# Performance work log

Measured on AMD Instinct MI355X. Metric: run time of the kernel, lower is better.

The kernel has to match this reference:

```python
import jax, jax.numpy as jnp
import numpy as np
from jax import lax

HEADS = 8
HEAD_C = 16  # attention_channels // heads = 128 // 8


def setup_inputs() -> dict:
    key = jax.random.key(0)
    ks = jax.random.split(key, 16)
    N, I, H, W = 8, 128, 36, 36
    R, C, A, O = 128, 128, 128, 128  # recurrent, common, attention, out channels
    s = lambda *sh: 0.05
    inp = {
        'x': jax.random.normal(ks[0], (N, I, H, W), jnp.float32),
        # input 1x1 conv (Accumulate of single Conv, bias init 0)
        'w_in': jax.random.normal(ks[1], (R, I), jnp.float32) * 0.05,
        'b_in': jnp.zeros((R,), jnp.float32),
        # 3x3 conv on cat([x, h]) -> common channels
        'w_conv': jax.random.normal(ks[2], (C, 2 * R, 3, 3), jnp.float32) * 0.05,
        'b_conv': jnp.zeros((C,), jnp.float32),
        # q/k/v 1x1 projections (no bias)
        'wq': jax.random.normal(ks[3], (A, C), jnp.float32) * 0.05,
        'wk': jax.random.normal(ks[4], (A, C), jnp.float32) * 0.05,
        'wv': jax.random.normal(ks[5], (A, C), jnp.float32) * 0.05,
        # gate 1x1 projections on cat([z, a]) (C + A inputs)
        'w_i': jax.random.normal(ks[6], (R, C + A), jnp.float32) * 0.05,
        'b_i': jnp.full((R,), -1.0, jnp.float32),  # init_input
        'w_f': jax.random.normal(ks[7], (R, C + A), jnp.float32) * 0.05,
        'b_f': jnp.full((R,), 1.0, jnp.float32),   # init_forget
        'w_g': jax.random.normal(ks[8], (R, C + A), jnp.float32) * 0.05,
        'b_g': jnp.zeros((R,), jnp.float32),
        'w_o': jax.random.normal(ks[9], (R, C + A), jnp.float32) * 0.05,
        'b_o': jnp.zeros((R,), jnp.float32),
        # output 1x1 conv
        'w_out': jax.random.normal(ks[10], (O, R), jnp.float32) * 0.05,
        'b_out': jnp.zeros((O,), jnp.float32),
    }
    return inp


def _conv1x1(w, x, b=None):
    y = jnp.einsum('oi,nihw->nohw', w, x)
    if b is not None:
        y = y + b[None, :, None, None]
    return y


def reference(x, w_in, b_in, w_conv, b_conv, wq, wk, wv,
              w_i, b_i, w_f, b_f, w_g, b_g, w_o, b_o, w_out, b_out):
    # first timestep: past is empty -> h = c = 0
    xt = jnp.tanh(_conv1x1(w_in, x, b_in))          # [N, R, H, W]
    h0 = jnp.zeros_like(xt)
    c0 = jnp.zeros_like(xt)
    xh = jnp.concatenate([xt, h0], axis=1)          # groups=1 -> plain concat
    z = lax.conv_general_dilated(xh, w_conv, (1, 1), 'SAME') + b_conv[None, :, None, None]
    N, C, H, W = z.shape
    HW = H * W
    q = _conv1x1(wq, z).reshape(N, HEADS, HEAD_C, HW)
    k = _conv1x1(wk, z).reshape(N, HEADS, HEAD_C, HW)
    v = _conv1x1(wv, z).reshape(N, HEADS, HEAD_C, HW)
    # spatial attention over H*W tokens per head
    w_attn = jax.nn.softmax(jnp.einsum('nhcq,nhcd->nhqd', q, k), axis=-1)  # [N,heads,HW,HW]
    a = jnp.einsum('nhcd,nhqd->nhcq', v, w_attn).reshape(N, -1, H, W)      # [N,A,H,W]
    za = jnp.concatenate([z, a], axis=1)
    i = jax.nn.sigmoid(_conv1x1(w_i, za, b_i))
    f = jax.nn.sigmoid(_conv1x1(w_f, za, b_f))
    g = jnp.tanh(_conv1x1(w_g, za, b_g))
    o = jax.nn.sigmoid(_conv1x1(w_o, za, b_o))
    c = f * c0 + i * g
    h = o * jnp.tanh(c)  # dropout p=0 -> identity
    return _conv1x1(w_out, h, b_out)
```

## Files before the change

kernel.cpp:

```cpp
#include <hip/hip_runtime.h>
#include <hip/hip_bf16.h>
#include <math.h>

typedef __hip_bfloat16 bf16;
typedef __attribute__((ext_vector_type(8))) short frag8;
typedef __attribute__((ext_vector_type(4))) float f32x4;
typedef __attribute__((ext_vector_type(16))) float f32x16;
typedef __attribute__((ext_vector_type(2))) unsigned int u32x2;
typedef __attribute__((ext_vector_type(4))) unsigned int u32x4;

#define HW  1296
#define CH  128
#define TT  1327104

__device__ __forceinline__ float b2f(bf16 v) { return __bfloat162float(v); }
__device__ __forceinline__ float bits2f(unsigned short u) {
    return __uint_as_float(((unsigned)u) << 16);
}
__device__ __forceinline__ float frcp(float x) { return __builtin_amdgcn_rcpf(x); }
__device__ __forceinline__ float fsigm(float x) { return frcp(1.0f + __expf(-x)); }
__device__ __forceinline__ float ftanh(float x) {
    float xc = fminf(15.0f, fmaxf(-15.0f, x));
    float e = __expf(2.0f * xc);
    return (e - 1.0f) * frcp(e + 1.0f);
}
__device__ __forceinline__ int packrh(float a, float b) {
    unsigned ua = __float_as_uint(a) + 0x8000u;
    unsigned ub = __float_as_uint(b) + 0x8000u;
    return (int)__builtin_amdgcn_perm(ub, ua, 0x07060302);
}
__device__ __forceinline__ int2 pack4(float a, float b, float c, float d) {
    int2 r; r.x = packrh(a, b); r.y = packrh(c, d); return r;
}
__device__ __forceinline__ unsigned cvtpk(float a, float b) {
    unsigned r;
    asm("v_cvt_pk_bf16_f32 %0, %1, %2" : "=v"(r) : "v"(a), "v"(b));
    return r;
}

__device__ __forceinline__ int detect_f32(const void* w) {
    const short4* p = (const short4*)w;
    short4 v = p[threadIdx.x & 63];
    int bad = 0;
    #pragma unroll
    for (int j = 0; j < 4; ++j) {
        float f = bits2f(((const unsigned short*)&v)[j]);
        if (!(fabsf(f) <= 100.0f)) bad = 1;
    }
    return __any(bad) ? 1 : 0;
}

__global__ __launch_bounds__(256) void k_prep(
    const void* w_in, const void* w_conv, const void* wq, const void* wk, const void* wv,
    const void* w_i, const void* w_g, const void* w_o, const void* w_out,
    const void* b_in, const void* b_conv, const void* b_i, const void* b_g,
    const void* b_o, const void* b_out,
    bf16* __restrict__ Wdst, float* __restrict__ Bdst)
{
    int idx = blockIdx.x * 256 + threadIdx.x;
    const int f = detect_f32(w_in);
    if (idx < 327680) {
        const void* src; int si;
        if (idx < 16384)       { src = w_in; si = idx; }
        else if (idx < 163840) { int j = idx - 16384; int tap = j >> 14, rem = j & 16383;
                                 int o = rem >> 7, r = rem & 127;
                                 src = w_conv; si = o * 2304 + r * 9 + tap; }
        else if (idx < 212992) { int j = idx - 163840; int o = j >> 7, i = j & 127;
                                 int ws_ = o >> 7;
                                 src = ws_ == 0 ? wq : ws_ == 1 ? wk : wv;
                                 si = (o & 127) * 128 + i; }
        else if (idx < 311296) { int j = idx - 212992; int g = j >> 15, rem = j & 32767;
                                 int o = rem >> 8, k = rem & 255;
                                 src = g == 0 ? w_i : g == 1 ? w_g : w_o; si = o * 256 + k; }
        else                   { int j = idx - 311296; int o = j >> 7, i = j & 127;
                                 src = w_out; si = o * 128 + i; }
        float v = f ? ((const float*)src)[si] : b2f(((const bf16*)src)[si]);
        if (idx >= 163840 && idx < 180224) v *= 1.4426950408889634f;
        Wdst[idx] = __float2bfloat16(v);
    } else if (idx < 327680 + 768) {
        int j = idx - 327680; int b = j >> 7, e = j & 127;
        const void* src = b == 0 ? b_in : b == 1 ? b_conv : b == 2 ? b_i
                        : b == 3 ? b_g : b == 4 ? b_o : b_out;
        Bdst[j] = f ? ((const float*)src)[e] : b2f(((const bf16*)src)[e]);
    }
}

__global__ __launch_bounds__(256) void k_inm(const void* __restrict__ x,
                                             const void* __restrict__ wraw,
                                             const bf16* __restrict__ Wm,
                                             const float* __restrict__ bias,
                                             bf16* __restrict__ XT) {
    __shared__ short Xl[32][132];
    const int tid = threadIdx.x, wave = tid >> 6, lane = tid & 63;
    const int quad = lane >> 4, l16 = lane & 15;
    const int n = blockIdx.x;
    const int pbase = blockIdx.y * 32;
    const int obase = blockIdx.z * 32 + (wave & 1) * 16;
    const int pstrip = (wave >> 1) * 16;
    const int f = detect_f32(wraw);

    #pragma unroll
    for (int rep = 0; rep < 4; ++rep) {
        int u = tid + rep * 256;
        int i = u >> 3;
        int p4 = (u & 7) * 4;
        int p = pbase + p4;
        short4 s = {0, 0, 0, 0};
        if (p < HW) {
            size_t gi = (size_t)n * CH * HW + (size_t)i * HW + p;
            if (f) {
                float4 fv = *(const float4*)((const float*)x + gi);
                int2 pk = pack4(fv.x, fv.y, fv.z, fv.w);
                s = *(short4*)&pk;
            } else {
                s = *(const short4*)((const bf16*)x + gi);
            }
        }
        Xl[p4 + 0][i] = s.x; Xl[p4 + 1][i] = s.y;
        Xl[p4 + 2][i] = s.z; Xl[p4 + 3][i] = s.w;
    }
    __syncthreads();

    const int pl = pstrip + l16;
    f32x4 acc = {0.f, 0.f, 0.f, 0.f};
    #pragma unroll
    for (int kc = 0; kc < 4; ++kc) {
        int k = kc * 32 + quad * 8;
        short4 b0 = *(const short4*)&Xl[pl][k];
        short4 b1 = *(const short4*)&Xl[pl][k + 4];
        frag8 bf = {b0.x, b0.y, b0.z, b0.w, b1.x, b1.y, b1.z, b1.w};
        frag8 wf = *(const frag8*)&Wm[(obase + l16) * CH + k];
        acc = __builtin_amdgcn_mfma_f32_16x16x32_bf16(wf, bf, acc, 0, 0, 0);
    }

    int p = pbase + pstrip + l16;
    if (p < HW) {
        int og = obase + quad * 4;
        int2 pk = pack4(ftanh(acc[0] + bias[og + 0]), ftanh(acc[1] + bias[og + 1]),
                        ftanh(acc[2] + bias[og + 2]), ftanh(acc[3] + bias[og + 3]));
        *(int2*)((short*)XT + ((size_t)n * HW + p) * CH + og) = pk;
    }
}

template<int MODE>
__global__ __launch_bounds__(256) void k_mm(
    const bf16* __restrict__ Act, const bf16* __restrict__ Act2,
    const bf16* __restrict__ Wm, const float* __restrict__ bias,
    bf16* __restrict__ o0, bf16* __restrict__ o1, bf16* __restrict__ o2)
{
    constexpr int NW  = (MODE == 2) ? 3 : 1;
    constexpr int KW  = (MODE == 2) ? 256 : 128;
    const int tid = threadIdx.x, wave = tid >> 6, lane = tid & 63;
    const int quad = lane >> 4, l16 = lane & 15;
    const int ostrip = wave & 1, pstrip = wave >> 1;
    const int n = blockIdx.x;
    const int obase = blockIdx.z * 32 + ostrip * 16;
    const int pbase = blockIdx.y * 64 + pstrip * 32;
    const bf16* actn = Act + (size_t)n * HW * CH;
    const bool vtile = (MODE == 1) && (obase >= 256);

    const int p1 = pbase + l16, p2 = pbase + 16 + l16;
    const bool p1ok = p1 < HW, p2ok = p2 < HW;

    frag8 zf = {0, 0, 0, 0, 0, 0, 0, 0};
    f32x4 acc[NW][2];
    #pragma unroll
    for (int g = 0; g < NW; ++g) {
        acc[g][0] = (f32x4){0.f, 0.f, 0.f, 0.f};
        acc[g][1] = (f32x4){0.f, 0.f, 0.f, 0.f};
    }

    if (MODE == 0) {
        const int h1 = p1 / 36, w1 = p1 - h1 * 36;
        const int h2 = p2 / 36, w2 = p2 - h2 * 36;
        #pragma unroll
        for (int tap = 0; tap < 9; ++tap) {
            int dy = tap / 3 - 1, dx = tap - (tap / 3) * 3 - 1;
            bool ok1 = p1ok && (unsigned)(h1 + dy) < 36u && (unsigned)(w1 + dx) < 36u;
            bool ok2 = p2ok && (unsigned)(h2 + dy) < 36u && (unsigned)(w2 + dx) < 36u;
            int sh = dy * 36 + dx;
            const bf16* a1 = actn + (size_t)(p1 + sh) * CH + quad * 8;
            const bf16* a2 = actn + (size_t)(p2 + sh) * CH + quad * 8;
            const bf16* wp = Wm + tap * 16384 + (obase + l16) * CH + quad * 8;
            #pragma unroll
            for (int kc = 0; kc < 4; ++kc) {
                frag8 bf1 = zf, bf2 = zf;
                if (ok1) bf1 = *(const frag8*)&a1[kc * 32];
                if (ok2) bf2 = *(const frag8*)&a2[kc * 32];
                frag8 wf = *(const frag8*)&wp[kc * 32];
                acc[0][0] = __builtin_amdgcn_mfma_f32_16x16x32_bf16(wf, bf1, acc[0][0], 0, 0, 0);
                acc[0][1] = __builtin_amdgcn_mfma_f32_16x16x32_bf16(wf, bf2, acc[0][1], 0, 0, 0);
            }
        }
    } else {
        const bf16* act2n = (MODE == 2) ? Act2 + (size_t)n * HW * CH : nullptr;
        #pragma unroll
        for (int kc = 0; kc < KW / 32; ++kc) {
            const bf16* src = (MODE == 2 && kc >= 4) ? act2n : actn;
            int ko = (MODE == 2 ? (kc & 3) : kc) * 32 + quad * 8;
            frag8 bf1 = zf, bf2 = zf;
            if (p1ok) bf1 = *(const frag8*)&src[(size_t)p1 * CH + ko];
            if (p2ok) bf2 = *(const frag8*)&src[(size_t)p2 * CH + ko];
            #pragma unroll
            for (int g = 0; g < NW; ++g) {
                const bf16* wp = Wm + g * 32768 + (obase + l16) * KW + kc * 32 + quad * 8;
                frag8 wf = *(const frag8*)wp;
                if (vtile) {
                    acc[g][0] = __builtin_amdgcn_mfma_f32_16x16x32_bf16(bf1, wf, acc[g][0], 0, 0, 0);
                    acc[g][1] = __builtin_amdgcn_mfma_f32_16x16x32_bf16(bf2, wf, acc[g][1], 0, 0, 0);
                } else {
                    acc[g][0] = __builtin_amdgcn_mfma_f32_16x16x32_bf16(wf, bf1, acc[g][0], 0, 0, 0);
                    acc[g][1] = __builtin_amdgcn_mfma_f32_16x16x32_bf16(wf, bf2, acc[g][1], 0, 0, 0);
                }
            }
        }
    }

    if (vtile) {
        int ov = (obase - 256) + l16;
        #pragma unroll
        for (int pt = 0; pt < 2; ++pt) {
            int p4 = pbase + pt * 16 + quad * 4;
            if (p4 >= HW) continue;
            int2 pk = pack4(acc[0][pt][0], acc[0][pt][1], acc[0][pt][2], acc[0][pt][3]);
            *(int2*)((short*)o2 + ((size_t)n * CH + ov) * HW + p4) = pk;
        }
        return;
    }
    const int og = obase + quad * 4;
    #pragma unroll
    for (int pt = 0; pt < 2; ++pt) {
        int p = pbase + pt * 16 + l16;
        if (p >= HW) continue;
        size_t rowoff = ((size_t)n * HW + p) * CH;
        if (MODE == 0) {
            int2 pk = pack4(acc[0][pt][0] + bias[og + 0], acc[0][pt][1] + bias[og + 1],
                            acc[0][pt][2] + bias[og + 2], acc[0][pt][3] + bias[og + 3]);
            *(int2*)((short*)o0 + rowoff + og) = pk;
        } else if (MODE == 1) {
            int which = og >> 7, ol = og & 127;
            bf16* dst = which == 0 ? o0 : o1;
            size_t di = (((size_t)n * 8 + (ol >> 4)) * HW + p) * 16 + (ol & 15);
            int2 pk = pack4(acc[0][pt][0], acc[0][pt][1], acc[0][pt][2], acc[0][pt][3]);
            *(int2*)((short*)dst + di) = pk;
        } else {
            float hv[4];
            #pragma unroll
            for (int r = 0; r < 4; ++r) {
                int o = og + r;
                float iv = fsigm(acc[0][pt][r] + bias[o]);
                float gv = ftanh(acc[1][pt][r] + bias[128 + o]);
                float ov = fsigm(acc[2][pt][r] + bias[256 + o]);
                hv[r] = ov * ftanh(iv * gv);
            }
            int2 pk = pack4(hv[0], hv[1], hv[2], hv[3]);
            *(int2*)((short*)o0 + rowoff + og) = pk;
        }
    }
}

__global__ __launch_bounds__(256) void k_outm(const bf16* __restrict__ Hb,
                                              const bf16* __restrict__ Wm,
                                              const float* __restrict__ bias,
                                              void* __restrict__ out,
                                              const void* __restrict__ wraw) {
    const int tid = threadIdx.x, wave = tid >> 6, lane = tid & 63;
    const int quad = lane >> 4, l16 = lane & 15;
    const int pstrip = wave & 1, ostrip = wave >> 1;
    const int n = blockIdx.x;
    const int pbase = blockIdx.y * 32 + pstrip * 16;
    const int obase = blockIdx.z * 64 + ostrip * 32;
    if (pbase >= HW) return;
    const int f32f = detect_f32(wraw);
    const bf16* hn = Hb + (size_t)n * HW * CH;
    const int pa = pbase + l16;

    f32x4 acc0 = {0.f, 0.f, 0.f, 0.f}, acc1 = {0.f, 0.f, 0.f, 0.f};
    #pragma unroll
    for (int kc = 0; kc < 4; ++kc) {
        int ko = kc * 32 + quad * 8;
        frag8 af = *(const frag8*)&hn[(size_t)pa * CH + ko];
        frag8 b0 = *(const frag8*)&Wm[(obase + l16) * CH + ko];
        frag8 b1 = *(const frag8*)&Wm[(obase + 16 + l16) * CH + ko];
        acc0 = __builtin_amdgcn_mfma_f32_16x16x32_bf16(af, b0, acc0, 0, 0, 0);
        acc1 = __builtin_amdgcn_mfma_f32_16x16x32_bf16(af, b1, acc1, 0, 0, 0);
    }
    int p4 = pbase + quad * 4;
    #pragma unroll
    for (int ot = 0; ot < 2; ++ot) {
        int o = obase + ot * 16 + l16;
        f32x4 a = ot ? acc1 : acc0;
        float bv = bias[o];
        size_t di = ((size_t)n * CH + o) * HW + p4;
        if (f32f) {
            float4 fv = {a[0] + bv, a[1] + bv, a[2] + bv, a[3] + bv};
            *(float4*)&((float*)out)[di] = fv;
        } else {
            int2 pk = pack4(a[0] + bv, a[1] + bv, a[2] + bv, a[3] + bv);
            *(int2*)&((short*)out)[di] = pk;
        }
    }
}

__global__ __launch_bounds__(256) void k_attn(const bf16* __restrict__ Qg,
                                              const bf16* __restrict__ Kg,
                                              const bf16* __restrict__ Vcf,
                                              bf16* __restrict__ A) {
    const int tid = threadIdx.x;
    const int w = tid >> 6, lane = tid & 63;
    const int l32 = lane & 31, hi = lane >> 5;
    const int n = blockIdx.x;
    const int head = blockIdx.z;
    const int qb = blockIdx.y * 128 + w * 32;
    if (qb >= HW) return;
    const int qtok = qb + l32;

    const short* Qh = (const short*)Qg + ((size_t)(n * 8 + head)) * HW * 16;
    const short* Kh = (const short*)Kg + ((size_t)(n * 8 + head)) * HW * 16;
    const short* Vh = (const short*)Vcf + ((size_t)n * CH + head * 16) * HW;

    frag8 qf = {0, 0, 0, 0, 0, 0, 0, 0};
    if (qtok < HW) qf = *(const frag8*)&Qh[(size_t)qtok * 16 + hi * 8];

    const short one = (short)0x3F80;
    const frag8 vones = {one, one, one, one, one, one, one, one};
    const frag8 vzero = {0, 0, 0, 0, 0, 0, 0, 0};
    const frag8 vfill = (l32 == 16) ? vones : vzero;
    const bool vload = l32 < 16;
    const short* Vrow = Vh + (size_t)(vload ? l32 : 0) * HW;

    const f32x16 zero16 = {};
    f32x16 Oacc = {};

    auto KLD = [&](int dd) -> frag8 {
        return *(const frag8*)&Kh[(size_t)(dd + l32) * 16 + hi * 8];
    };
    auto VLD = [&](int dd) -> frag8 {
        return vload ? *(const frag8*)&Vrow[dd + hi * 8] : vfill;
    };

    frag8 kf = KLD(0);
    frag8 va = VLD(0), vb = VLD(16);

    for (int it = 0; it < 40; ++it) {
        const int d0 = it * 32;
        f32x16 S = __builtin_amdgcn_mfma_f32_32x32x16_bf16(kf, qf, zero16, 0, 0, 0);
        frag8 kn = KLD(d0 + 32);
        frag8 van = VLD(d0 + 32);
        frag8 vbn = VLD(d0 + 48);

        float p[16];
        #pragma unroll
        for (int r = 0; r < 16; ++r) p[r] = __builtin_amdgcn_exp2f(S[r]);

        #pragma unroll
        for (int hh = 0; hh < 2; ++hh) {
            unsigned P0 = cvtpk(p[hh * 8 + 0], p[hh * 8 + 1]);
            unsigned P1 = cvtpk(p[hh * 8 + 2], p[hh * 8 + 3]);
            unsigned P2 = cvtpk(p[hh * 8 + 4], p[hh * 8 + 5]);
            unsigned P3 = cvtpk(p[hh * 8 + 6], p[hh * 8 + 7]);
            u32x2 s02 = __builtin_amdgcn_permlane32_swap(P0, P2, false, false);
            u32x2 s13 = __builtin_amdgcn_permlane32_swap(P1, P3, false, false);
            u32x4 bw = {s02[0], s13[0], s02[1], s13[1]};
            frag8 pf = __builtin_bit_cast(frag8, bw);
            Oacc = __builtin_amdgcn_mfma_f32_32x32x16_bf16(hh ? vb : va, pf, Oacc, 0, 0, 0);
        }
        kf = kn; va = van; vb = vbn;
    }

    {
        f32x16 S = __builtin_amdgcn_mfma_f32_32x32x16_bf16(kf, qf, zero16, 0, 0, 0);
        float p[8];
        #pragma unroll
        for (int r = 0; r < 8; ++r) p[r] = __builtin_amdgcn_exp2f(S[r]);
        unsigned P0 = cvtpk(p[0], p[1]);
        unsigned P1 = cvtpk(p[2], p[3]);
        unsigned P2 = cvtpk(p[4], p[5]);
        unsigned P3 = cvtpk(p[6], p[7]);
        u32x2 s02 = __builtin_amdgcn_permlane32_swap(P0, P2, false, false);
        u32x2 s13 = __builtin_amdgcn_permlane32_swap(P1, P3, false, false);
        u32x4 bw = {s02[0], s13[0], s02[1], s13[1]};
        frag8 pf = __builtin_bit_cast(frag8, bw);
        Oacc = __builtin_amdgcn_mfma_f32_32x32x16_bf16(va, pf, Oacc, 0, 0, 0);
    }

    float lsum = Oacc[8];
    u32x2 lb = __builtin_amdgcn_permlane32_swap(__float_as_uint(lsum),
                                                __float_as_uint(lsum), false, false);
    float inv = frcp(__uint_as_float(lb[0]));

    if (qtok < HW) {
        short* An = (short*)A + ((size_t)n * HW + qtok) * CH + head * 16;
        int2 pk0 = pack4(Oacc[0] * inv, Oacc[1] * inv, Oacc[2] * inv, Oacc[3] * inv);
        int2 pk1 = pack4(Oacc[4] * inv, Oacc[5] * inv, Oacc[6] * inv, Oacc[7] * inv);
        *(int2*)&An[hi * 4] = pk0;
        *(int2*)&An[8 + hi * 4] = pk1;
    }
}

extern "C" void kernel_launch(void* const* d_in, const int* in_sizes, int n_in,
                              void* d_out, int out_size, void* d_ws, size_t ws_size,
                              hipStream_t stream) {
    char* ws = (char*)d_ws;
    bf16*  Wst  = (bf16*)(ws + 256);
    float* Bst  = (float*)(ws + 655616);
    bf16*  XT   = (bf16*)(ws + 1048576);
    bf16*  Zb   = XT + TT;
    bf16*  Qb   = Zb + TT;
    bf16*  Kb   = Qb + TT;
    bf16*  Vb   = Kb + TT;
    bf16*  Ab   = Vb + TT;
    bf16*  Hb   = Ab + TT;

    k_prep<<<1284, 256, 0, stream>>>(d_in[1], d_in[3], d_in[5], d_in[6], d_in[7],
                                     d_in[8], d_in[12], d_in[14], d_in[16],
                                     d_in[2], d_in[4], d_in[9], d_in[13], d_in[15], d_in[17],
                                     Wst, Bst);
    k_inm<<<dim3(8, 41, 4), 256, 0, stream>>>(d_in[0], d_in[1], Wst, Bst, XT);
    k_mm<0><<<dim3(8, 21, 4), 256, 0, stream>>>(XT, nullptr, Wst + 16384, Bst + 128,
                                                Zb, nullptr, nullptr);
    k_mm<1><<<dim3(8, 21, 12), 256, 0, stream>>>(Zb, nullptr, Wst + 163840, nullptr,
                                                 Qb, Kb, Vb);
    k_attn<<<dim3(8, 11, 8), 256, 0, stream>>>(Qb, Kb, Vb, Ab);
    k_mm<2><<<dim3(8, 21, 4), 256, 0, stream>>>(Zb, Ab, Wst + 212992, Bst + 256,
                                                Hb, nullptr, nullptr);
    k_outm<<<dim3(8, 41, 2), 256, 0, stream>>>(Hb, Wst + 311296, Bst + 640, d_out, d_in[1]);
}
```

Measured before the change: 200.9 us.

## Split attention key range across two wave groups and halve matmul pixel tiles

The attention kernel now launches 512 threads per block. Two groups of four waves each process half of the key range, and their partial outputs and row sums are merged through shared memory before normalisation. The S matmul for the next chunk is issued one iteration ahead to overlap with the exp/PV work. The k_mm kernels drop from 32 to 16 pixels per wave and launch twice as many blocks along the pixel axis, raising parallelism at the cost of less weight-fragment reuse per load.

```diff
diff --git a/kernel.cpp b/kernel.cpp
--- a/kernel.cpp
+++ b/kernel.cpp
@@ -155,41 +155,33 @@
     const int ostrip = wave & 1, pstrip = wave >> 1;
     const int n = blockIdx.x;
     const int obase = blockIdx.z * 32 + ostrip * 16;
-    const int pbase = blockIdx.y * 64 + pstrip * 32;
+    const int pbase = blockIdx.y * 32 + pstrip * 16;
     const bf16* actn = Act + (size_t)n * HW * CH;
     const bool vtile = (MODE == 1) && (obase >= 256);
 
-    const int p1 = pbase + l16, p2 = pbase + 16 + l16;
-    const bool p1ok = p1 < HW, p2ok = p2 < HW;
+    const int p1 = pbase + l16;
+    const bool p1ok = p1 < HW;
 
     frag8 zf = {0, 0, 0, 0, 0, 0, 0, 0};
-    f32x4 acc[NW][2];
-    #pragma unroll
-    for (int g = 0; g < NW; ++g) {
-        acc[g][0] = (f32x4){0.f, 0.f, 0.f, 0.f};
-        acc[g][1] = (f32x4){0.f, 0.f, 0.f, 0.f};
-    }
+    f32x4 acc[NW];
+    #pragma unroll
+    for (int g = 0; g < NW; ++g) acc[g] = (f32x4){0.f, 0.f, 0.f, 0.f};
 
     if (MODE == 0) {
         const int h1 = p1 / 36, w1 = p1 - h1 * 36;
-        const int h2 = p2 / 36, w2 = p2 - h2 * 36;
         #pragma unroll
         for (int tap = 0; tap < 9; ++tap) {
             int dy = tap / 3 - 1, dx = tap - (tap / 3) * 3 - 1;
             bool ok1 = p1ok && (unsigned)(h1 + dy) < 36u && (unsigned)(w1 + dx) < 36u;
-            bool ok2 = p2ok && (unsigned)(h2 + dy) < 36u && (unsigned)(w2 + dx) < 36u;
             int sh = dy * 36 + dx;
             const bf16* a1 = actn + (size_t)(p1 + sh) * CH + quad * 8;
-            const bf16* a2 = actn + (size_t)(p2 + sh) * CH + quad * 8;
             const bf16* wp = Wm + tap * 16384 + (obase + l16) * CH + quad * 8;
             #pragma unroll
             for (int kc = 0; kc < 4; ++kc) {
-                frag8 bf1 = zf, bf2 = zf;
+                frag8 bf1 = zf;
                 if (ok1) bf1 = *(const frag8*)&a1[kc * 32];
-                if (ok2) bf2 = *(const frag8*)&a2[kc * 32];
                 frag8 wf = *(const frag8*)&wp[kc * 32];
-                acc[0][0] = __builtin_amdgcn_mfma_f32_16x16x32_bf16(wf, bf1, acc[0][0], 0, 0, 0);
-                acc[0][1] = __builtin_amdgcn_mfma_f32_16x16x32_bf16(wf, bf2, acc[0][1], 0, 0, 0);
+                acc[0] = __builtin_amdgcn_mfma_f32_16x16x32_bf16(wf, bf1, acc[0], 0, 0, 0);
             }
         }
     } else {
@@ -198,19 +190,16 @@
         for (int kc = 0; kc < KW / 32; ++kc) {
             const bf16* src = (MODE == 2 && kc >= 4) ? act2n : actn;
             int ko = (MODE == 2 ? (kc & 3) : kc) * 32 + quad * 8;
-            frag8 bf1 = zf, bf2 = zf;
+            frag8 bf1 = zf;
             if (p1ok) bf1 = *(const frag8*)&src[(size_t)p1 * CH + ko];
-            if (p2ok) bf2 = *(const frag8*)&src[(size_t)p2 * CH + ko];
             #pragma unroll
             for (int g = 0; g < NW; ++g) {
                 const bf16* wp = Wm + g * 32768 + (obase + l16) * KW + kc * 32 + quad * 8;
                 frag8 wf = *(const frag8*)wp;
                 if (vtile) {
-                    acc[g][0] = __builtin_amdgcn_mfma_f32_16x16x32_bf16(bf1, wf, acc[g][0], 0, 0, 0);
-                    acc[g][1] = __builtin_amdgcn_mfma_f32_16x16x32_bf16(bf2, wf, acc[g][1], 0, 0, 0);
+                    acc[g] = __builtin_amdgcn_mfma_f32_16x16x32_bf16(bf1, wf, acc[g], 0, 0, 0);
                 } else {
-                    acc[g][0] = __builtin_amdgcn_mfma_f32_16x16x32_bf16(wf, bf1, acc[g][0], 0, 0, 0);
-                    acc[g][1] = __builtin_amdgcn_mfma_f32_16x16x32_bf16(wf, bf2, acc[g][1], 0, 0, 0);
+                    acc[g] = __builtin_amdgcn_mfma_f32_16x16x32_bf16(wf, bf1, acc[g], 0, 0, 0);
                 }
             }
         }
@@ -218,44 +207,39 @@
 
     if (vtile) {
         int ov = (obase - 256) + l16;
-        #pragma unroll
-        for (int pt = 0; pt < 2; ++pt) {
-            int p4 = pbase + pt * 16 + quad * 4;
-            if (p4 >= HW) continue;
-            int2 pk = pack4(acc[0][pt][0], acc[0][pt][1], acc[0][pt][2], acc[0][pt][3]);
+        int p4 = pbase + quad * 4;
+        if (p4 < HW) {
+            int2 pk = pack4(acc[0][0], acc[0][1], acc[0][2], acc[0][3]);
             *(int2*)((short*)o2 + ((size_t)n * CH + ov) * HW + p4) = pk;
         }
         return;
     }
     const int og = obase + quad * 4;
-    #pragma unroll
-    for (int pt = 0; pt < 2; ++pt) {
-        int p = pbase + pt * 16 + l16;
-        if (p >= HW) continue;
-        size_t rowoff = ((size_t)n * HW + p) * CH;
-        if (MODE == 0) {
-            int2 pk = pack4(acc[0][pt][0] + bias[og + 0], acc[0][pt][1] + bias[og + 1],
-                            acc[0][pt][2] + bias[og + 2], acc[0][pt][3] + bias[og + 3]);
-            *(int2*)((short*)o0 + rowoff + og) = pk;
-        } else if (MODE == 1) {
-            int which = og >> 7, ol = og & 127;
-            bf16* dst = which == 0 ? o0 : o1;
-            size_t di = (((size_t)n * 8 + (ol >> 4)) * HW + p) * 16 + (ol & 15);
-            int2 pk = pack4(acc[0][pt][0], acc[0][pt][1], acc[0][pt][2], acc[0][pt][3]);
-            *(int2*)((short*)dst + di) = pk;
-        } else {
-            float hv[4];
-            #pragma unroll
-            for (int r = 0; r < 4; ++r) {
-                int o = og + r;
-                float iv = fsigm(acc[0][pt][r] + bias[o]);
-                float gv = ftanh(acc[1][pt][r] + bias[128 + o]);
-                float ov = fsigm(acc[2][pt][r] + bias[256 + o]);
-                hv[r] = ov * ftanh(iv * gv);
-            }
-            int2 pk = pack4(hv[0], hv[1], hv[2], hv[3]);
-            *(int2*)((short*)o0 + rowoff + og) = pk;
-        }
+    const int p = pbase + l16;
+    if (p >= HW) return;
+    size_t rowoff = ((size_t)n * HW + p) * CH;
+    if (MODE == 0) {
+        int2 pk = pack4(acc[0][0] + bias[og + 0], acc[0][1] + bias[og + 1],
+                        acc[0][2] + bias[og + 2], acc[0][3] + bias[og + 3]);
+        *(int2*)((short*)o0 + rowoff + og) = pk;
+    } else if (MODE == 1) {
+        int which = og >> 7, ol = og & 127;
+        bf16* dst = which == 0 ? o0 : o1;
+        size_t di = (((size_t)n * 8 + (ol >> 4)) * HW + p) * 16 + (ol & 15);
+        int2 pk = pack4(acc[0][0], acc[0][1], acc[0][2], acc[0][3]);
+        *(int2*)((short*)dst + di) = pk;
+    } else {
+        float hv[4];
+        #pragma unroll
+        for (int r = 0; r < 4; ++r) {
+            int o = og + r;
+            float iv = fsigm(acc[0][r] + bias[o]);
+            float gv = ftanh(acc[1][r] + bias[128 + o]);
+            float ov = fsigm(acc[2][r] + bias[256 + o]);
+            hv[r] = ov * ftanh(iv * gv);
+        }
+        int2 pk = pack4(hv[0], hv[1], hv[2], hv[3]);
+        *(int2*)((short*)o0 + rowoff + og) = pk;
     }
 }
 
@@ -302,17 +286,19 @@
     }
 }
 
-__global__ __launch_bounds__(256) void k_attn(const bf16* __restrict__ Qg,
+__global__ __launch_bounds__(512) void k_attn(const bf16* __restrict__ Qg,
                                               const bf16* __restrict__ Kg,
                                               const bf16* __restrict__ Vcf,
                                               bf16* __restrict__ A) {
+    __shared__ float Lc[4][9][64];
+
     const int tid = threadIdx.x;
     const int w = tid >> 6, lane = tid & 63;
     const int l32 = lane & 31, hi = lane >> 5;
+    const int qw = w & 3, dq = w >> 2;
     const int n = blockIdx.x;
     const int head = blockIdx.z;
-    const int qb = blockIdx.y * 128 + w * 32;
-    if (qb >= HW) return;
+    const int qb = blockIdx.y * 128 + qw * 32;
     const int qtok = qb + l32;
 
     const short* Qh = (const short*)Qg + ((size_t)(n * 8 + head)) * HW * 16;
@@ -339,15 +325,19 @@
         return vload ? *(const frag8*)&Vrow[dd + hi * 8] : vfill;
     };
 
-    frag8 kf = KLD(0);
-    frag8 va = VLD(0), vb = VLD(16);
-
-    for (int it = 0; it < 40; ++it) {
-        const int d0 = it * 32;
-        f32x16 S = __builtin_amdgcn_mfma_f32_32x32x16_bf16(kf, qf, zero16, 0, 0, 0);
-        frag8 kn = KLD(d0 + 32);
+    const int c0 = dq ? 20 : 0;
+    frag8 kf  = KLD(c0 * 32);
+    frag8 kf2 = KLD(c0 * 32 + 32);
+    frag8 va  = VLD(c0 * 32);
+    frag8 vb  = VLD(c0 * 32 + 16);
+    f32x16 S = __builtin_amdgcn_mfma_f32_32x32x16_bf16(kf, qf, zero16, 0, 0, 0);
+
+    for (int it = 0; it < 20; ++it) {
+        const int d0 = (c0 + it) * 32;
+        frag8 kn  = KLD(d0 + 64);
         frag8 van = VLD(d0 + 32);
         frag8 vbn = VLD(d0 + 48);
+        f32x16 Sn = __builtin_amdgcn_mfma_f32_32x32x16_bf16(kf2, qf, zero16, 0, 0, 0);
 
         float p[16];
         #pragma unroll
@@ -365,11 +355,10 @@
             frag8 pf = __builtin_bit_cast(frag8, bw);
             Oacc = __builtin_amdgcn_mfma_f32_32x32x16_bf16(hh ? vb : va, pf, Oacc, 0, 0, 0);
         }
-        kf = kn; va = van; vb = vbn;
-    }
-
-    {
-        f32x16 S = __builtin_amdgcn_mfma_f32_32x32x16_bf16(kf, qf, zero16, 0, 0, 0);
+        kf2 = kn; va = van; vb = vbn; S = Sn;
+    }
+
+    if (dq) {
         float p[8];
         #pragma unroll
         for (int r = 0; r < 8; ++r) p[r] = __builtin_amdgcn_exp2f(S[r]);
@@ -382,19 +371,25 @@
         u32x4 bw = {s02[0], s13[0], s02[1], s13[1]};
         frag8 pf = __builtin_bit_cast(frag8, bw);
         Oacc = __builtin_amdgcn_mfma_f32_32x32x16_bf16(va, pf, Oacc, 0, 0, 0);
-    }
-
-    float lsum = Oacc[8];
-    u32x2 lb = __builtin_amdgcn_permlane32_swap(__float_as_uint(lsum),
-                                                __float_as_uint(lsum), false, false);
-    float inv = frcp(__uint_as_float(lb[0]));
-
-    if (qtok < HW) {
-        short* An = (short*)A + ((size_t)n * HW + qtok) * CH + head * 16;
-        int2 pk0 = pack4(Oacc[0] * inv, Oacc[1] * inv, Oacc[2] * inv, Oacc[3] * inv);
-        int2 pk1 = pack4(Oacc[4] * inv, Oacc[5] * inv, Oacc[6] * inv, Oacc[7] * inv);
-        *(int2*)&An[hi * 4] = pk0;
-        *(int2*)&An[8 + hi * 4] = pk1;
+        #pragma unroll
+        for (int r = 0; r < 8; ++r) Lc[qw][r][lane] = Oacc[r];
+        Lc[qw][8][lane] = Oacc[8];
+    }
+    __syncthreads();
+    if (dq == 0) {
+        #pragma unroll
+        for (int r = 0; r < 8; ++r) Oacc[r] += Lc[qw][r][lane];
+        float lsum = Oacc[8] + Lc[qw][8][lane];
+        u32x2 lb = __builtin_amdgcn_permlane32_swap(__float_as_uint(lsum),
+                                                    __float_as_uint(lsum), false, false);
+        float inv = frcp(__uint_as_float(lb[0]));
+        if (qtok < HW) {
+            short* An = (short*)A + ((size_t)n * HW + qtok) * CH + head * 16;
+            int2 pk0 = pack4(Oacc[0] * inv, Oacc[1] * inv, Oacc[2] * inv, Oacc[3] * inv);
+            int2 pk1 = pack4(Oacc[4] * inv, Oacc[5] * inv, Oacc[6] * inv, Oacc[7] * inv);
+            *(int2*)&An[hi * 4] = pk0;
+            *(int2*)&An[8 + hi * 4] = pk1;
+        }
     }
 }
 
@@ -417,12 +412,12 @@
                                      d_in[2], d_in[4], d_in[9], d_in[13], d_in[15], d_in[17],
                                      Wst, Bst);
     k_inm<<<dim3(8, 41, 4), 256, 0, stream>>>(d_in[0], d_in[1], Wst, Bst, XT);
-    k_mm<0><<<dim3(8, 21, 4), 256, 0, stream>>>(XT, nullptr, Wst + 16384, Bst + 128,
+    k_mm<0><<<dim3(8, 41, 4), 256, 0, stream>>>(XT, nullptr, Wst + 16384, Bst + 128,
                                                 Zb, nullptr, nullptr);
-    k_mm<1><<<dim3(8, 21, 12), 256, 0, stream>>>(Zb, nullptr, Wst + 163840, nullptr,
+    k_mm<1><<<dim3(8, 41, 12), 256, 0, stream>>>(Zb, nullptr, Wst + 163840, nullptr,
                                                  Qb, Kb, Vb);
-    k_attn<<<dim3(8, 11, 8), 256, 0, stream>>>(Qb, Kb, Vb, Ab);
-    k_mm<2><<<dim3(8, 21, 4), 256, 0, stream>>>(Zb, Ab, Wst + 212992, Bst + 256,
+    k_attn<<<dim3(8, 11, 8), 512, 0, stream>>>(Qb, Kb, Vb, Ab);
+    k_mm<2><<<dim3(8, 41, 4), 256, 0, stream>>>(Zb, Ab, Wst + 212992, Bst + 256,
                                                 Hb, nullptr, nullptr);
     k_outm<<<dim3(8, 41, 2), 256, 0, stream>>>(Hb, Wst + 311296, Bst + 640, d_out, d_in[1]);
 }
```

Measured after the change: 219.5 us. 1.09x slower.
